# Kernel tuning notes

Hardware: AMD Instinct MI355X
Metric: run time of the kernel (lower is better)

## Reference

```python
import jax, jax.numpy as jnp
import numpy as np

SCALE = 64.0
MARGIN = 0.5
ALPHA = 1.2
SIGMA = 2.0
THRESH = float(np.cos(np.pi - MARGIN))
MM = float(np.sin(np.pi - MARGIN) * MARGIN)
IN_F, OUT_F, BATCH = 512, 100000, 512


def setup_inputs() -> dict:
    key = jax.random.key(0)
    k1, k2, k3 = jax.random.split(key, 3)
    x = jax.random.normal(k1, (BATCH, IN_F), dtype=jnp.float32)
    label = jax.random.randint(k2, (BATCH,), 0, OUT_F, dtype=jnp.int64 if jax.config.read('jax_enable_x64') else jnp.int32)
    stdv = 1.0 / np.sqrt(IN_F)
    weight = jax.random.uniform(k3, (OUT_F, IN_F), dtype=jnp.float32, minval=-stdv, maxval=stdv)
    return {"input": x, "label": label, "weight": weight}


def reference(input, label, weight):
    # row-normalize embeddings and class weights
    ex = input / jnp.linalg.norm(input, axis=1, keepdims=True)
    ew = weight / jnp.linalg.norm(weight, axis=1, keepdims=True)
    cos = jnp.einsum('bd,cd->bc', ex, ew)  # [B, C]

    b = jnp.arange(cos.shape[0])
    cos_lb = cos[b, label]  # [B] cosine at the true class
    # arcface margin: cos(theta + m) above thresh, linear fallback below
    target = jnp.where(cos_lb > THRESH,
                       jnp.cos(jnp.arccos(cos_lb) + MARGIN),
                       cos_lb - MM)  # [B]

    # negative reweighting: gaussian around the margined target (detached)
    t_scale = ALPHA * jnp.exp(-jnp.square(cos - target[:, None]) / SIGMA)
    t_scale = jax.lax.stop_gradient(t_scale)

    onehot = jax.nn.one_hot(label, cos.shape[1], dtype=cos.dtype)  # a_scale; c_scale = 1 - onehot
    logits = SCALE * (onehot * target[:, None]
                      + (1.0 - onehot) * (t_scale * cos + t_scale - 1.0))
    return logits
```

## Files before the change

### kernel.cpp

```cpp
#include <hip/hip_runtime.h>
#include <hip/hip_bf16.h>

typedef unsigned short ushort_t;
typedef unsigned int uint_t;

typedef __attribute__((ext_vector_type(8))) short short8;
typedef __attribute__((ext_vector_type(4))) float f32x4;

#define BATCH 512
#define DK    512
#define CTOT  100000
#define BN    64
#define THRESH_C (-0.8775825618903728f)
#define MM_C     (0.2397127693021015f)

static __device__ __forceinline__ ushort_t f2bf(float f) {
    union { float f; uint_t u; } v; v.f = f;
    return (ushort_t)((v.u + 0x7FFFu + ((v.u >> 16) & 1u)) >> 16);
}

__global__ __launch_bounds__(256) void arc_prep(
    const float* __restrict__ x, const int* __restrict__ label,
    const float* __restrict__ w, float* __restrict__ target,
    ushort_t* __restrict__ exbF)
{
    const int b = blockIdx.x;
    const int t = threadIdx.x;
    __shared__ float red[8];

    const float2 xv = ((const float2*)(x + (size_t)b * DK))[t];
    float ss = xv.x * xv.x + xv.y * xv.y;
    #pragma unroll
    for (int o = 32; o; o >>= 1) ss += __shfl_xor(ss, o);
    if ((t & 63) == 0) red[t >> 6] = ss;
    __syncthreads();
    const float ssx = red[0] + red[1] + red[2] + red[3];
    const float rnx = 1.0f / sqrtf(ssx);

    {
        const int k = 2 * t;
        const int ko = k >> 5;
        const int qk = (k >> 3) & 3;
        const int kj = k & 7;
        const size_t F = (size_t)(b >> 4) * 8192 + (size_t)ko * 512
                       + (size_t)qk * 128 + (size_t)(b & 15) * 8 + kj;
        ushort2 e;
        e.x = f2bf(xv.x * rnx);
        e.y = f2bf(xv.y * rnx);
        *(ushort2*)(exbF + F) = e;
    }

    const int lb = label[b];
    const float2 wv = ((const float2*)(w + (size_t)lb * DK))[t];
    float ssw = wv.x * wv.x + wv.y * wv.y;
    float dot = xv.x * wv.x + xv.y * wv.y;
    #pragma unroll
    for (int o = 32; o; o >>= 1) { ssw += __shfl_xor(ssw, o); dot += __shfl_xor(dot, o); }
    __syncthreads();
    if ((t & 63) == 0) { red[t >> 6] = ssw; red[4 + (t >> 6)] = dot; }
    __syncthreads();
    if (t == 0) {
        const float sw = red[0] + red[1] + red[2] + red[3];
        const float dt = red[4] + red[5] + red[6] + red[7];
        float cl = dt * rnx / sqrtf(sw);
        cl = fminf(fmaxf(cl, -1.0f), 1.0f);
        const float tg = (cl > THRESH_C) ? cosf(acosf(cl) + 0.5f) : (cl - MM_C);
        target[b] = tg;
    }
}

__global__ __launch_bounds__(512, 4) void arc_main(
    const ushort_t* __restrict__ exbF, const float* __restrict__ w,
    const int* __restrict__ label, const float* __restrict__ target,
    float* __restrict__ out)
{
    __shared__ ushort_t Bs[BN * DK];

    const int t    = threadIdx.x;
    const int lane = t & 63;
    const int wid  = t >> 6;
    const int c0   = blockIdx.x * BN;

    const int br  = t >> 3;
    const int bj  = t & 7;
    const int cls = c0 + br;
    const bool valid = (cls < CTOT);
    const float* wrow = w + (size_t)cls * DK;
    const int s3 = br & 7;
    float bsq = 0.0f;
    #pragma unroll
    for (int i = 0; i < 16; ++i) {
        const int c = i * 32 + bj * 4;
        float4 q = valid ? *(const float4*)(wrow + c)
                         : make_float4(0.f, 0.f, 0.f, 0.f);
        bsq += q.x * q.x + q.y * q.y + q.z * q.z + q.w * q.w;
        uint2 p;
        p.x = (uint_t)f2bf(q.x) | ((uint_t)f2bf(q.y) << 16);
        p.y = (uint_t)f2bf(q.z) | ((uint_t)f2bf(q.w) << 16);
        const int k16 = c >> 3;
        const int sw  = k16 ^ s3;
        *(uint2*)&Bs[br * DK + sw * 8 + (bj & 1) * 4] = p;
    }
    bsq += __shfl_xor(bsq, 1);
    bsq += __shfl_xor(bsq, 2);
    bsq += __shfl_xor(bsq, 4);
    __syncthreads();

    const int m0   = wid * 64;
    const int colq = lane & 15;
    const int qk   = lane >> 4;
    const int bs3  = colq & 7;
    const ushort_t* abase = exbF + (size_t)(wid * 4) * 8192 + (size_t)lane * 8;

    f32x4 acc[4][4];
    #pragma unroll
    for (int i = 0; i < 4; ++i)
        #pragma unroll
        for (int j = 0; j < 4; ++j)
            acc[i][j] = (f32x4){0.f, 0.f, 0.f, 0.f};

    #pragma unroll 2
    for (int ko = 0; ko < 16; ++ko) {
        short8 bfr[4];
        #pragma unroll
        for (int nt = 0; nt < 4; ++nt) {
            const int idx = (nt * 16 + colq) * DK + (((ko << 2) | qk) ^ bs3) * 8;
            bfr[nt] = *(const short8*)&Bs[idx];
        }
        #pragma unroll
        for (int mt = 0; mt < 4; ++mt) {
            const short8 afr = *(const short8*)(abase + (size_t)mt * 8192 + ko * 512);
            #pragma unroll
            for (int nt = 0; nt < 4; ++nt)
                acc[mt][nt] = __builtin_amdgcn_mfma_f32_16x16x32_bf16(afr, bfr[nt], acc[mt][nt], 0, 0, 0);
        }
    }

    __syncthreads();
    if ((t & 7) == 0) ((float*)Bs)[br] = valid ? (1.0f / sqrtf(bsq)) : 0.0f;
    __syncthreads();
    float rn[4];
    #pragma unroll
    for (int nt = 0; nt < 4; ++nt) rn[nt] = ((float*)Bs)[nt * 16 + colq];

    #pragma unroll
    for (int mt = 0; mt < 4; ++mt) {
        #pragma unroll
        for (int rr = 0; rr < 4; ++rr) {
            const int row = m0 + mt * 16 + qk * 4 + rr;
            const float tg = target[row];
            const int   lb = label[row];
            float* orow = out + (size_t)row * CTOT + c0;
            #pragma unroll
            for (int nt = 0; nt < 4; ++nt) {
                const int cc = c0 + nt * 16 + colq;
                if (cc >= CTOT) continue;
                const float cosv = acc[mt][nt][rr] * rn[nt];
                const float d  = cosv - tg;
                const float ts = 1.2f * __expf(d * d * -0.5f);
                const float v  = (cc == lb) ? 64.0f * tg
                                            : 64.0f * (ts * cosv + ts - 1.0f);
                orow[nt * 16 + colq] = v;
            }
        }
    }
}

extern "C" void kernel_launch(void* const* d_in, const int* in_sizes, int n_in,
                              void* d_out, int out_size, void* d_ws, size_t ws_size,
                              hipStream_t stream) {
    const float* x     = (const float*)d_in[0];
    const int*   label = (const int*)d_in[1];
    const float* w     = (const float*)d_in[2];
    float* out = (float*)d_out;

    float*    target = (float*)d_ws;
    ushort_t* exbF   = (ushort_t*)((char*)d_ws + 2048);

    arc_prep<<<512, 256, 0, stream>>>(x, label, w, target, exbF);

    const int nblk = (CTOT + BN - 1) / BN;
    arc_main<<<nblk, 512, 0, stream>>>(exbF, w, label, target, out);
}
```

Before: 415.3 us.

## Load weight fragments directly from global memory, dropping LDS staging

```diff
diff --git a/kernel.cpp b/kernel.cpp
--- a/kernel.cpp
+++ b/kernel.cpp
@@ -10,7 +10,8 @@
 #define BATCH 512
 #define DK    512
 #define CTOT  100000
-#define BN    64
+#define CPAD  100032
+#define BNF   64
 #define THRESH_C (-0.8775825618903728f)
 #define MM_C     (0.2397127693021015f)
 
@@ -69,47 +70,19 @@
     }
 }
 
-__global__ __launch_bounds__(512, 4) void arc_main(
+__global__ __launch_bounds__(512, 4) void arc_main_f(
     const ushort_t* __restrict__ exbF, const float* __restrict__ w,
     const int* __restrict__ label, const float* __restrict__ target,
     float* __restrict__ out)
 {
-    __shared__ ushort_t Bs[BN * DK];
-
     const int t    = threadIdx.x;
     const int lane = t & 63;
     const int wid  = t >> 6;
-    const int c0   = blockIdx.x * BN;
-
-    const int br  = t >> 3;
-    const int bj  = t & 7;
-    const int cls = c0 + br;
-    const bool valid = (cls < CTOT);
-    const float* wrow = w + (size_t)cls * DK;
-    const int s3 = br & 7;
-    float bsq = 0.0f;
-    #pragma unroll
-    for (int i = 0; i < 16; ++i) {
-        const int c = i * 32 + bj * 4;
-        float4 q = valid ? *(const float4*)(wrow + c)
-                         : make_float4(0.f, 0.f, 0.f, 0.f);
-        bsq += q.x * q.x + q.y * q.y + q.z * q.z + q.w * q.w;
-        uint2 p;
-        p.x = (uint_t)f2bf(q.x) | ((uint_t)f2bf(q.y) << 16);
-        p.y = (uint_t)f2bf(q.z) | ((uint_t)f2bf(q.w) << 16);
-        const int k16 = c >> 3;
-        const int sw  = k16 ^ s3;
-        *(uint2*)&Bs[br * DK + sw * 8 + (bj & 1) * 4] = p;
-    }
-    bsq += __shfl_xor(bsq, 1);
-    bsq += __shfl_xor(bsq, 2);
-    bsq += __shfl_xor(bsq, 4);
-    __syncthreads();
-
-    const int m0   = wid * 64;
+    const int tile = blockIdx.x;
+    const int c0   = tile * BNF;
     const int colq = lane & 15;
     const int qk   = lane >> 4;
-    const int bs3  = colq & 7;
+
     const ushort_t* abase = exbF + (size_t)(wid * 4) * 8192 + (size_t)lane * 8;
 
     f32x4 acc[4][4];
@@ -119,51 +92,90 @@
         for (int j = 0; j < 4; ++j)
             acc[i][j] = (f32x4){0.f, 0.f, 0.f, 0.f};
 
-    #pragma unroll 2
-    for (int ko = 0; ko < 16; ++ko) {
-        short8 bfr[4];
-        #pragma unroll
-        for (int nt = 0; nt < 4; ++nt) {
-            const int idx = (nt * 16 + colq) * DK + (((ko << 2) | qk) ^ bs3) * 8;
-            bfr[nt] = *(const short8*)&Bs[idx];
-        }
-        #pragma unroll
-        for (int mt = 0; mt < 4; ++mt) {
-            const short8 afr = *(const short8*)(abase + (size_t)mt * 8192 + ko * 512);
-            #pragma unroll
-            for (int nt = 0; nt < 4; ++nt)
-                acc[mt][nt] = __builtin_amdgcn_mfma_f32_16x16x32_bf16(afr, bfr[nt], acc[mt][nt], 0, 0, 0);
-        }
+    float ss[4] = {0.f, 0.f, 0.f, 0.f};
+
+#define KLOOP(GUARD)                                                           \
+    {                                                                          \
+        const float* wl[4];                                                    \
+        bool vm[4];                                                            \
+        _Pragma("unroll")                                                      \
+        for (int nt = 0; nt < 4; ++nt) {                                       \
+            const int cls = c0 + nt * 16 + colq;                               \
+            vm[nt] = !GUARD || (cls < CTOT);                                   \
+            wl[nt] = w + (size_t)(vm[nt] ? cls : 0) * DK + qk * 8;             \
+        }                                                                      \
+        _Pragma("unroll 2")                                                    \
+        for (int ko = 0; ko < 16; ++ko) {                                      \
+            short8 bfr[4];                                                     \
+            _Pragma("unroll")                                                  \
+            for (int nt = 0; nt < 4; ++nt) {                                   \
+                const float* wp = wl[nt] + ko * 32;                            \
+                float4 q0 = *(const float4*)wp;                                \
+                float4 q1 = *(const float4*)(wp + 4);                          \
+                if (GUARD && !vm[nt]) {                                        \
+                    q0 = make_float4(0.f, 0.f, 0.f, 0.f); q1 = q0;             \
+                }                                                              \
+                ss[nt] += q0.x * q0.x + q0.y * q0.y + q0.z * q0.z + q0.w * q0.w\
+                        + q1.x * q1.x + q1.y * q1.y + q1.z * q1.z + q1.w * q1.w;\
+                union { short8 s; uint4 u; } bb;                               \
+                bb.u.x = (uint_t)f2bf(q0.x) | ((uint_t)f2bf(q0.y) << 16);      \
+                bb.u.y = (uint_t)f2bf(q0.z) | ((uint_t)f2bf(q0.w) << 16);      \
+                bb.u.z = (uint_t)f2bf(q1.x) | ((uint_t)f2bf(q1.y) << 16);      \
+                bb.u.w = (uint_t)f2bf(q1.z) | ((uint_t)f2bf(q1.w) << 16);      \
+                bfr[nt] = bb.s;                                                \
+            }                                                                  \
+            _Pragma("unroll")                                                  \
+            for (int mt = 0; mt < 4; ++mt) {                                   \
+                const short8 afr = *(const short8*)(abase + (size_t)mt * 8192  \
+                                                    + ko * 512);               \
+                _Pragma("unroll")                                              \
+                for (int nt = 0; nt < 4; ++nt)                                 \
+                    acc[mt][nt] = __builtin_amdgcn_mfma_f32_16x16x32_bf16(     \
+                        afr, bfr[nt], acc[mt][nt], 0, 0, 0);                   \
+            }                                                                  \
+        }                                                                      \
     }
 
-    __syncthreads();
-    if ((t & 7) == 0) ((float*)Bs)[br] = valid ? (1.0f / sqrtf(bsq)) : 0.0f;
-    __syncthreads();
+    const bool full = (c0 + BNF <= CTOT);
+    if (full) { KLOOP(false) } else { KLOOP(true) }
+#undef KLOOP
+
     float rn[4];
     #pragma unroll
-    for (int nt = 0; nt < 4; ++nt) rn[nt] = ((float*)Bs)[nt * 16 + colq];
+    for (int nt = 0; nt < 4; ++nt) {
+        float s = ss[nt];
+        s += __shfl_xor(s, 16);
+        s += __shfl_xor(s, 32);
+        rn[nt] = 1.0f / sqrtf(s);
+    }
 
-    #pragma unroll
-    for (int mt = 0; mt < 4; ++mt) {
-        #pragma unroll
-        for (int rr = 0; rr < 4; ++rr) {
-            const int row = m0 + mt * 16 + qk * 4 + rr;
-            const float tg = target[row];
-            const int   lb = label[row];
-            float* orow = out + (size_t)row * CTOT + c0;
-            #pragma unroll
-            for (int nt = 0; nt < 4; ++nt) {
-                const int cc = c0 + nt * 16 + colq;
-                if (cc >= CTOT) continue;
-                const float cosv = acc[mt][nt][rr] * rn[nt];
-                const float d  = cosv - tg;
-                const float ts = 1.2f * __expf(d * d * -0.5f);
-                const float v  = (cc == lb) ? 64.0f * tg
-                                            : 64.0f * (ts * cosv + ts - 1.0f);
-                orow[nt * 16 + colq] = v;
-            }
-        }
+    const int m0 = wid * 64;
+
+#define EPILOGUE(GUARD)                                                        \
+    _Pragma("unroll")                                                          \
+    for (int mt = 0; mt < 4; ++mt) {                                           \
+        _Pragma("unroll")                                                      \
+        for (int rr = 0; rr < 4; ++rr) {                                       \
+            const int row = m0 + mt * 16 + qk * 4 + rr;                        \
+            const float tg = target[row];                                      \
+            const int   lb = label[row];                                       \
+            float* orow = out + (size_t)row * CTOT + c0;                       \
+            _Pragma("unroll")                                                  \
+            for (int nt = 0; nt < 4; ++nt) {                                   \
+                const int cc = c0 + nt * 16 + colq;                            \
+                if (GUARD && cc >= CTOT) continue;                             \
+                const float cosv = acc[mt][nt][rr] * rn[nt];                   \
+                const float d  = cosv - tg;                                    \
+                const float ts = 1.2f * __expf(d * d * -0.5f);                 \
+                const float v  = (cc == lb) ? 64.0f * tg                       \
+                                            : 64.0f * (ts * cosv + ts - 1.0f); \
+                orow[nt * 16 + colq] = v;                                      \
+            }                                                                  \
+        }                                                                      \
     }
+
+    if (full) { EPILOGUE(false) } else { EPILOGUE(true) }
+#undef EPILOGUE
 }
 
 extern "C" void kernel_launch(void* const* d_in, const int* in_sizes, int n_in,
@@ -178,7 +190,5 @@
     ushort_t* exbF   = (ushort_t*)((char*)d_ws + 2048);
 
     arc_prep<<<512, 256, 0, stream>>>(x, label, w, target, exbF);
-
-    const int nblk = (CTOT + BN - 1) / BN;
-    arc_main<<<nblk, 512, 0, stream>>>(exbF, w, label, target, out);
+    arc_main_f<<<CPAD / BNF, 512, 0, stream>>>(exbF, w, label, target, out);
 }
```

After: 568.5 us. 1.37x slower.

## Stage epilogue through LDS for float4 nontemporal stores and fragment-order weight staging

Applied to the files above, without the earlier changes.

```diff
diff --git a/kernel.cpp b/kernel.cpp
--- a/kernel.cpp
+++ b/kernel.cpp
@@ -10,7 +10,8 @@
 #define BATCH 512
 #define DK    512
 #define CTOT  100000
-#define BN    64
+#define CPAD  100032
+#define BNF   64
 #define THRESH_C (-0.8775825618903728f)
 #define MM_C     (0.2397127693021015f)
 
@@ -69,47 +70,66 @@
     }
 }
 
-__global__ __launch_bounds__(512, 4) void arc_main(
+__global__ __launch_bounds__(512, 4) void arc_fused(
     const ushort_t* __restrict__ exbF, const float* __restrict__ w,
     const int* __restrict__ label, const float* __restrict__ target,
     float* __restrict__ out)
 {
-    __shared__ ushort_t Bs[BN * DK];
+    __shared__ ushort_t Bs[4 * 8192];
+    __shared__ float    rsum[8 * 64];
 
     const int t    = threadIdx.x;
     const int lane = t & 63;
     const int wid  = t >> 6;
-    const int c0   = blockIdx.x * BN;
-
-    const int br  = t >> 3;
-    const int bj  = t & 7;
-    const int cls = c0 + br;
-    const bool valid = (cls < CTOT);
-    const float* wrow = w + (size_t)cls * DK;
-    const int s3 = br & 7;
-    float bsq = 0.0f;
-    #pragma unroll
-    for (int i = 0; i < 16; ++i) {
-        const int c = i * 32 + bj * 4;
-        float4 q = valid ? *(const float4*)(wrow + c)
-                         : make_float4(0.f, 0.f, 0.f, 0.f);
-        bsq += q.x * q.x + q.y * q.y + q.z * q.z + q.w * q.w;
-        uint2 p;
-        p.x = (uint_t)f2bf(q.x) | ((uint_t)f2bf(q.y) << 16);
-        p.y = (uint_t)f2bf(q.z) | ((uint_t)f2bf(q.w) << 16);
-        const int k16 = c >> 3;
-        const int sw  = k16 ^ s3;
-        *(uint2*)&Bs[br * DK + sw * 8 + (bj & 1) * 4] = p;
-    }
-    bsq += __shfl_xor(bsq, 1);
-    bsq += __shfl_xor(bsq, 2);
-    bsq += __shfl_xor(bsq, 4);
-    __syncthreads();
-
-    const int m0   = wid * 64;
+    const int tile = blockIdx.x;
+    const int c0   = tile * BNF;
     const int colq = lane & 15;
     const int qk   = lane >> 4;
-    const int bs3  = colq & 7;
+
+    {
+        float ssr[4] = {0.f, 0.f, 0.f, 0.f};
+        #pragma unroll
+        for (int i = 0; i < 8; ++i) {
+            const int rb  = i >> 1;
+            const int ko  = (i & 1) * 8 + wid;
+            const int row = c0 + rb * 16 + colq;
+            const float* src = w + (size_t)row * DK + ko * 32 + qk * 8;
+            f32x4 q0 = (f32x4){0.f, 0.f, 0.f, 0.f};
+            f32x4 q1 = q0;
+            if (row < CTOT) {
+                q0 = __builtin_nontemporal_load((const f32x4*)src);
+                q1 = __builtin_nontemporal_load((const f32x4*)(src + 4));
+            }
+            ssr[rb] += q0.x * q0.x + q0.y * q0.y + q0.z * q0.z + q0.w * q0.w
+                     + q1.x * q1.x + q1.y * q1.y + q1.z * q1.z + q1.w * q1.w;
+            uint4 p;
+            p.x = (uint_t)f2bf(q0.x) | ((uint_t)f2bf(q0.y) << 16);
+            p.y = (uint_t)f2bf(q0.z) | ((uint_t)f2bf(q0.w) << 16);
+            p.z = (uint_t)f2bf(q1.x) | ((uint_t)f2bf(q1.y) << 16);
+            p.w = (uint_t)f2bf(q1.z) | ((uint_t)f2bf(q1.w) << 16);
+            *(uint4*)&Bs[i * 4096 + t * 8] = p;
+        }
+        #pragma unroll
+        for (int rb = 0; rb < 4; ++rb) {
+            ssr[rb] += __shfl_xor(ssr[rb], 16);
+            ssr[rb] += __shfl_xor(ssr[rb], 32);
+        }
+        if (lane < 16) {
+            #pragma unroll
+            for (int rb = 0; rb < 4; ++rb)
+                rsum[wid * 64 + rb * 16 + lane] = ssr[rb];
+        }
+    }
+
+    __syncthreads();
+
+    if (t < 64) {
+        float s = 0.f;
+        #pragma unroll
+        for (int wv = 0; wv < 8; ++wv) s += rsum[wv * 64 + t];
+        rsum[t] = (c0 + t < CTOT) ? (1.0f / sqrtf(s)) : 0.0f;
+    }
+
     const ushort_t* abase = exbF + (size_t)(wid * 4) * 8192 + (size_t)lane * 8;
 
     f32x4 acc[4][4];
@@ -119,29 +139,34 @@
         for (int j = 0; j < 4; ++j)
             acc[i][j] = (f32x4){0.f, 0.f, 0.f, 0.f};
 
+    const ushort_t* bbase = Bs + (size_t)lane * 8;
     #pragma unroll 2
     for (int ko = 0; ko < 16; ++ko) {
-        short8 bfr[4];
-        #pragma unroll
-        for (int nt = 0; nt < 4; ++nt) {
-            const int idx = (nt * 16 + colq) * DK + (((ko << 2) | qk) ^ bs3) * 8;
-            bfr[nt] = *(const short8*)&Bs[idx];
-        }
-        #pragma unroll
-        for (int mt = 0; mt < 4; ++mt) {
-            const short8 afr = *(const short8*)(abase + (size_t)mt * 8192 + ko * 512);
+        short8 bfr[4], afr[4];
+        #pragma unroll
+        for (int nt = 0; nt < 4; ++nt)
+            bfr[nt] = *(const short8*)(bbase + nt * 8192 + ko * 512);
+        #pragma unroll
+        for (int mt = 0; mt < 4; ++mt)
+            afr[mt] = *(const short8*)(abase + (size_t)mt * 8192 + ko * 512);
+        #pragma unroll
+        for (int mt = 0; mt < 4; ++mt)
             #pragma unroll
             for (int nt = 0; nt < 4; ++nt)
-                acc[mt][nt] = __builtin_amdgcn_mfma_f32_16x16x32_bf16(afr, bfr[nt], acc[mt][nt], 0, 0, 0);
-        }
-    }
-
-    __syncthreads();
-    if ((t & 7) == 0) ((float*)Bs)[br] = valid ? (1.0f / sqrtf(bsq)) : 0.0f;
-    __syncthreads();
+                acc[mt][nt] = __builtin_amdgcn_mfma_f32_16x16x32_bf16(
+                    afr[mt], bfr[nt], acc[mt][nt], 0, 0, 0);
+    }
+
+    __syncthreads();
+
     float rn[4];
     #pragma unroll
-    for (int nt = 0; nt < 4; ++nt) rn[nt] = ((float*)Bs)[nt * 16 + colq];
+    for (int nt = 0; nt < 4; ++nt) rn[nt] = rsum[nt * 16 + colq];
+
+    float* Ts = (float*)Bs + wid * (16 * 67);
+
+    const int  m0   = wid * 64;
+    const bool full = (c0 + BNF <= CTOT);
 
     #pragma unroll
     for (int mt = 0; mt < 4; ++mt) {
@@ -150,19 +175,34 @@
             const int row = m0 + mt * 16 + qk * 4 + rr;
             const float tg = target[row];
             const int   lb = label[row];
-            float* orow = out + (size_t)row * CTOT + c0;
             #pragma unroll
             for (int nt = 0; nt < 4; ++nt) {
                 const int cc = c0 + nt * 16 + colq;
-                if (cc >= CTOT) continue;
                 const float cosv = acc[mt][nt][rr] * rn[nt];
                 const float d  = cosv - tg;
                 const float ts = 1.2f * __expf(d * d * -0.5f);
                 const float v  = (cc == lb) ? 64.0f * tg
                                             : 64.0f * (ts * cosv + ts - 1.0f);
-                orow[nt * 16 + colq] = v;
+                Ts[(qk * 4 + rr) * 67 + nt * 16 + colq] = v;
             }
         }
+        asm volatile("s_waitcnt lgkmcnt(0)" ::: "memory");
+
+        #pragma unroll
+        for (int i = 0; i < 4; ++i) {
+            const int r16 = i * 4 + qk;
+            const int row = m0 + mt * 16 + r16;
+            const int cc4 = 4 * colq;
+            f32x4 v;
+            v.x = Ts[r16 * 67 + cc4 + 0];
+            v.y = Ts[r16 * 67 + cc4 + 1];
+            v.z = Ts[r16 * 67 + cc4 + 2];
+            v.w = Ts[r16 * 67 + cc4 + 3];
+            if (full || (c0 + cc4 < CTOT))
+                __builtin_nontemporal_store(
+                    v, (f32x4*)(out + (size_t)row * CTOT + c0 + cc4));
+        }
+        asm volatile("s_waitcnt lgkmcnt(0)" ::: "memory");
     }
 }
 
@@ -178,7 +218,5 @@
     ushort_t* exbF   = (ushort_t*)((char*)d_ws + 2048);
 
     arc_prep<<<512, 256, 0, stream>>>(x, label, w, target, exbF);
-
-    const int nblk = (CTOT + BN - 1) / BN;
-    arc_main<<<nblk, 512, 0, stream>>>(exbF, w, label, target, out);
-}
+    arc_fused<<<CPAD / BNF, 512, 0, stream>>>(exbF, w, label, target, out);
+}
```

Result: faster. 393.9 us (-5.1%).
